# Performance work log

Measured on AMD Instinct MI355X. Metric: run time of the kernel, lower is better.

Reference implementation:

```python
import jax, jax.numpy as jnp
import numpy as np

N_NODES = 100
F_IN = 65536
C_OUT = 60
ACTION_DIM = 100
N_EDGES = 2000


def setup_inputs() -> dict:
    key = jax.random.key(0)
    ks = jax.random.split(key, 16)
    s = 0.02
    return {
        "substrate_features": jax.random.normal(ks[0], (1, N_NODES, F_IN), jnp.float32),
        "edge_index": jax.random.randint(ks[1], (2, N_EDGES), 0, N_NODES, dtype=jnp.int32),
        "v_cpu_demand_t": jax.random.uniform(ks[2], (1,), jnp.float32),
        "v_bw_demand_t": jax.random.uniform(ks[3], (1,), jnp.float32),
        "num_pending_v_nodes_t": jax.random.uniform(ks[4], (1,), jnp.float32),
        "actor_w": jax.random.normal(ks[5], (3, F_IN, C_OUT), jnp.float32) * s,
        "actor_b": jax.random.normal(ks[6], (C_OUT,), jnp.float32) * s,
        "critic_w": jax.random.normal(ks[7], (3, F_IN, C_OUT), jnp.float32) * s,
        "critic_b": jax.random.normal(ks[8], (C_OUT,), jnp.float32) * s,
        "actor_fc_w": jax.random.normal(ks[9], (N_NODES * C_OUT + 3, ACTION_DIM), jnp.float32) * s,
        "actor_fc_b": jax.random.normal(ks[10], (ACTION_DIM,), jnp.float32) * s,
        "critic_fc_w": jax.random.normal(ks[11], (N_NODES * C_OUT + 3, 1), jnp.float32) * s,
        "critic_fc_b": jax.random.normal(ks[12], (1,), jnp.float32) * s,
    }


def cheb_conv(x, edge_index, W, b):
    # ChebConv, K=3, sym normalization, lambda_max=2 (PyG defaults).
    # With lambda_max=2 the scaled Laplacian is L_hat = -D^{-1/2} A D^{-1/2}
    # (diagonal becomes 0 after the -1 self-loop shift).
    # x: [1, N, F]; edge_index: [2, E]; W: [3, F, C]; b: [C]
    src, dst = edge_index[0], edge_index[1]
    n = x.shape[1]
    deg = jax.ops.segment_sum(jnp.ones(src.shape[0], x.dtype), src, num_segments=n)
    dis = jnp.where(deg > 0, jax.lax.rsqrt(jnp.where(deg > 0, deg, 1.0)), 0.0)
    norm = -(dis[src] * dis[dst])  # [E], L_hat off-diagonal entries
    x2 = x[0]  # [N, F]

    def prop(z):  # z: [N, F] -> L_hat @ z via gather/scatter over edges
        return jax.ops.segment_sum(z[src] * norm[:, None], dst, num_segments=n)

    Tx0 = x2
    Tx1 = prop(Tx0)
    Tx2 = 2.0 * prop(Tx1) - Tx0
    out = Tx0 @ W[0] + Tx1 @ W[1] + Tx2 @ W[2] + b  # [N, C]
    return out[None]  # [1, N, C]


def reference(substrate_features, edge_index, v_cpu_demand_t, v_bw_demand_t,
              num_pending_v_nodes_t, actor_w, actor_b, critic_w, critic_b,
              actor_fc_w, actor_fc_b, critic_fc_w, critic_fc_b):
    emb_a = jnp.tanh(cheb_conv(substrate_features, edge_index, actor_w, actor_b))
    emb_a = emb_a.reshape(1, -1)  # [1, N*60]
    emb_c = jnp.tanh(cheb_conv(substrate_features, edge_index, critic_w, critic_b))
    emb_c = emb_c.reshape(1, -1)
    extras = [v_cpu_demand_t[None], v_bw_demand_t[None], num_pending_v_nodes_t[None]]  # each [1,1]
    state_a = jnp.concatenate([emb_a] + extras, axis=1)  # [1, 6003]
    state_c = jnp.concatenate([emb_c] + extras, axis=1)
    logits = state_a @ actor_fc_w + actor_fc_b  # [1, action_dim]
    values = state_c @ critic_fc_w + critic_fc_b  # [1, 1]
    return (logits, values)
```

## Files before the change

kernel.cpp:

```cpp
#include <hip/hip_runtime.h>
#include <stdint.h>

#define F_IN 65536
#define NN 100
#define CO 60
#define G_SPLIT 128
#define KC (F_IN/G_SPLIT)
#define BK 32
#define NIT (KC/BK)
#define NBUF 3
#define ABYTES (112*BK*2)
#define WBYTES (BK*CO*4)
#define BUFB (ABYTES+WBYTES)

typedef short v8s __attribute__((ext_vector_type(8)));
typedef float v4f __attribute__((ext_vector_type(4)));

__device__ __forceinline__ unsigned int f2bf(float x){
  unsigned int u = __float_as_uint(x);
  u += 0x7fffu + ((u>>16)&1u);
  return u>>16;
}
__device__ __forceinline__ v4f mfma16(v8s a, v8s b, v4f c){
  return __builtin_amdgcn_mfma_f32_16x16x32_bf16(a,b,c,0,0,0);
}
__device__ __forceinline__ void cp16(const void* g, void* l){
  __builtin_amdgcn_global_load_lds((const __attribute__((address_space(1))) void*)g,
                                   (__attribute__((address_space(3))) void*)l, 16, 0, 0);
}

__global__ __launch_bounds__(256)
void k_cvt(const float* __restrict__ x, unsigned short* __restrict__ xb){
  int i = blockIdx.x*256 + threadIdx.x;
  float4 v = ((const float4*)x)[i];
  uint2 w;
  w.x = f2bf(v.x) | (f2bf(v.y)<<16);
  w.y = f2bf(v.z) | (f2bf(v.w)<<16);
  ((uint2*)xb)[i] = w;
}

__global__ __launch_bounds__(256,3)
void k_gemm(const unsigned short* __restrict__ xb, const float* __restrict__ aw,
            const float* __restrict__ cw, float* __restrict__ dst, int partial){
  const int s = blockIdx.x, g = blockIdx.y;
  const int k0 = s*KC;
  const int tid = threadIdx.x, wave = tid>>6, lane = tid&63, quad = lane>>4, nl = lane&15;
  const int c0 = wave*16, ccl = min(c0+nl, CO-1);

  __shared__ __align__(16) char S[NBUF*BUFB];

  const float* W = (g<3) ? (aw + (size_t)g*F_IN*CO) : (cw + (size_t)(g-3)*F_IN*CO);

  const char* gsrc[4]; unsigned ldst[4]; unsigned gstep[4];
  #pragma unroll
  for(int i=0;i<4;++i){
    int id = wave*4 + i;
    if(id >= 15) id = 0;
    if(id < 7){
      int t = id;
      int row = t*16 + (lane>>2);
      int rcl = min(row, NN-1);
      int lch = (lane&3) ^ (row&3);
      gsrc[i]  = (const char*)(xb + (size_t)rcl*F_IN + k0) + lch*16;
      gstep[i] = BK*2;
      ldst[i]  = t*1024 + lane*16;
    } else {
      int t = id - 7;
      int off = t*1024; if(off > WBYTES-1024) off = WBYTES-1024;
      gsrc[i]  = (const char*)W + (size_t)k0*CO*4 + off + lane*16;
      gstep[i] = WBYTES;
      ldst[i]  = ABYTES + off + lane*16;
    }
  }

  v4f acc[7];
  #pragma unroll
  for(int i=0;i<7;++i){ v4f z={0.f,0.f,0.f,0.f}; acc[i]=z; }

  #define ISSUE(it) { char* b_ = S + ((it)%NBUF)*BUFB; \
    _Pragma("unroll") for(int i_=0;i_<4;++i_) cp16(gsrc[i_] + (size_t)(it)*gstep[i_], b_ + ldst[i_]); }

  #define COMPUTE(it) { const char* b_ = S + ((it)%NBUF)*BUFB; \
    const unsigned short* Ab_ = (const unsigned short*)b_; \
    const float* Wb_ = (const float*)(b_ + ABYTES); \
    v8s fB_; \
    _Pragma("unroll") for(int j_=0;j_<8;++j_) fB_[j_] = (short)f2bf(Wb_[(quad*8+j_)*CO + ccl]); \
    _Pragma("unroll") for(int mt_=0;mt_<7;++mt_){ \
      int r_ = mt_*16 + nl; \
      v8s a_ = *(const v8s*)(Ab_ + r_*BK + ((quad ^ (r_&3))*8)); \
      acc[mt_] = mfma16(a_, fB_, acc[mt_]); } }

  ISSUE(0); ISSUE(1);
  for(int it=0; it<NIT-1; ++it){
    __builtin_amdgcn_sched_barrier(0);
    asm volatile("s_waitcnt vmcnt(4)" ::: "memory");
    __builtin_amdgcn_s_barrier();
    __builtin_amdgcn_sched_barrier(0);
    if(it+2 < NIT) ISSUE(it+2);
    COMPUTE(it);
  }
  __builtin_amdgcn_sched_barrier(0);
  asm volatile("s_waitcnt vmcnt(0)" ::: "memory");
  __builtin_amdgcn_s_barrier();
  __builtin_amdgcn_sched_barrier(0);
  COMPUTE(NIT-1);

  const int c = c0 + nl;
  if(c < CO){
    if(partial){
      float* pd = dst + ((size_t)g*G_SPLIT + s)*(NN*CO);
      #pragma unroll
      for(int mt=0;mt<7;++mt){
        #pragma unroll
        for(int i=0;i<4;++i){
          int m = mt*16 + quad*4 + i;
          if(m < NN) pd[m*CO + c] = acc[mt][i];
        }
      }
    } else {
      float* pd = dst + (size_t)g*(NN*CO);
      #pragma unroll
      for(int mt=0;mt<7;++mt){
        #pragma unroll
        for(int i=0;i<4;++i){
          int m = mt*16 + quad*4 + i;
          if(m < NN) atomicAdd(pd + m*CO + c, acc[mt][i]);
        }
      }
    }
  }
}

__global__ void k_reduce(const float* __restrict__ P, float* __restrict__ Y){
  int o = blockIdx.x*256 + threadIdx.x;
  if(o >= 6*NN*CO) return;
  int gg = o/(NN*CO), r = o - gg*(NN*CO);
  const float* p = P + (size_t)gg*G_SPLIT*(NN*CO) + (size_t)blockIdx.y*32*(NN*CO) + r;
  float a0=0.f,a1=0.f,a2=0.f,a3=0.f;
  #pragma unroll 2
  for(int s4=0;s4<32;s4+=4){
    a0 += p[(s4  )*(NN*CO)];
    a1 += p[(s4+1)*(NN*CO)];
    a2 += p[(s4+2)*(NN*CO)];
    a3 += p[(s4+3)*(NN*CO)];
  }
  atomicAdd(&Y[o], (a0+a1)+(a2+a3));
}

__global__ void k_cheb(const float* __restrict__ Y, const int* __restrict__ ei,
                       const float* __restrict__ ab, const float* __restrict__ cb,
                       float* __restrict__ emb){
  const int net = blockIdx.x / CO;
  const int c   = blockIdx.x % CO;
  const int t   = threadIdx.x;
  __shared__ float L[NN][NN+1];
  __shared__ float dis[NN];
  __shared__ int   deg[NN];
  __shared__ float y0[NN], y1[NN], y2[NN], zu[NN];

  for(int i=t;i<NN*(NN+1);i+=128) ((float*)L)[i]=0.f;
  if(t<NN) deg[t]=0;
  __syncthreads();
  for(int e=t;e<2000;e+=128) atomicAdd(&deg[ei[e]],1);
  __syncthreads();
  if(t<NN) dis[t] = deg[t]>0 ? rsqrtf((float)deg[t]) : 0.f;
  __syncthreads();
  for(int e=t;e<2000;e+=128){
    int s = ei[e], d = ei[2000+e];
    atomicAdd(&L[d][s], -dis[s]*dis[d]);
  }
  if(t<NN){
    const float* yb = Y + (size_t)net*3*NN*CO + t*CO + c;
    y0[t]=yb[0]; y1[t]=yb[NN*CO]; y2[t]=yb[2*NN*CO];
  }
  __syncthreads();
  if(t<NN){
    float s=0.f;
    #pragma unroll 4
    for(int j=0;j<NN;++j) s += L[t][j]*y2[j];
    zu[t] = y1[t] + 2.f*s;
  }
  __syncthreads();
  if(t<NN){
    float s=0.f;
    #pragma unroll 4
    for(int j=0;j<NN;++j) s += L[t][j]*zu[j];
    float b = (net==0) ? ab[c] : cb[c];
    emb[net*NN*CO + t*CO + c] = tanhf(y0[t] - y2[t] + s + b);
  }
}

#define FCB 25
__global__ void k_fc(const float* __restrict__ emb, const float* __restrict__ afw,
                     const float* __restrict__ afb, const float* __restrict__ cfw,
                     const float* __restrict__ cfb, const float* __restrict__ s0,
                     const float* __restrict__ s1, const float* __restrict__ s2,
                     float* __restrict__ out){
  const int b = blockIdx.x;
  const int t = threadIdx.x;
  if(b < FCB){
    const int jj = t & 127, half = t >> 7;
    if(jj < 100){
      const int i0 = b*240 + half*120;
      const float* w = afw + (size_t)i0*100 + jj;
      const float* e = emb + i0;
      float p = 0.f;
      #pragma unroll 4
      for(int i=0;i<120;++i) p += e[i]*w[(size_t)i*100];
      atomicAdd(&out[jj], p);
    }
  } else {
    float p = 0.f;
    const float* e = emb + 6000;
    for(int i=t;i<6000;i+=256) p += e[i]*cfw[i];
    #pragma unroll
    for(int o=32;o>0;o>>=1) p += __shfl_down(p,o,64);
    __shared__ float red[4];
    if((t&63)==0) red[t>>6]=p;
    __syncthreads();
    if(t==0){
      float tot = red[0]+red[1]+red[2]+red[3];
      out[100] = tot + s0[0]*cfw[6000] + s1[0]*cfw[6001] + s2[0]*cfw[6002] + cfb[0];
    }
    if(t<100){
      atomicAdd(&out[t], afb[t] + s0[0]*afw[600000+t] + s1[0]*afw[600100+t] + s2[0]*afw[600200+t]);
    }
  }
}

extern "C" void kernel_launch(void* const* d_in, const int* in_sizes, int n_in,
                              void* d_out, int out_size, void* d_ws, size_t ws_size,
                              hipStream_t stream){
  const float* x   = (const float*)d_in[0];
  const int*   ei  = (const int*)d_in[1];
  const float* s0  = (const float*)d_in[2];
  const float* s1  = (const float*)d_in[3];
  const float* s2  = (const float*)d_in[4];
  const float* aw  = (const float*)d_in[5];
  const float* ab  = (const float*)d_in[6];
  const float* cw  = (const float*)d_in[7];
  const float* cb  = (const float*)d_in[8];
  const float* afw = (const float*)d_in[9];
  const float* afb = (const float*)d_in[10];
  const float* cfw = (const float*)d_in[11];
  const float* cfb = (const float*)d_in[12];
  float* out = (float*)d_out;

  unsigned short* xb = (unsigned short*)d_ws;
  float* Y   = (float*)((char*)d_ws + 13107200);
  float* emb = Y + 6*NN*CO;
  float* P   = emb + 2*NN*CO;
  const size_t need_full = 13107200u + (size_t)(6*NN*CO + 2*NN*CO)*4 + (size_t)6*G_SPLIT*NN*CO*4;
  const int partial = (ws_size >= need_full) ? 1 : 0;

  hipMemsetAsync(Y, 0, 6*NN*CO*sizeof(float), stream);
  hipMemsetAsync(out, 0, 101*sizeof(float), stream);

  k_cvt<<<6400, 256, 0, stream>>>(x, xb);
  k_gemm<<<dim3(G_SPLIT,6), 256, 0, stream>>>(xb, aw, cw, partial ? P : Y, partial);
  if(partial){
    k_reduce<<<dim3((6*NN*CO+255)/256, 4), 256, 0, stream>>>(P, Y);
  }
  k_cheb<<<120, 128, 0, stream>>>(Y, ei, ab, cb, emb);
  k_fc<<<FCB+1, 256, 0, stream>>>(emb, afw, afb, cfw, cfb, s0, s1, s2, out);
}
```

Before: 218.8 us.

## Replace LDS-staged GEMM pipeline with direct global loads and double the K split

Drops the triple-buffered global_load_lds staging of activations and weights in the split-K GEMM. Each lane now loads its A fragments and W column values straight from global memory into registers. The K split doubles to 256 slices, so twice as many blocks each run a shorter loop, occupancy hint rises to 4, and the reduce grid grows to match. This removes LDS traffic and barriers, but gives up explicit prefetch and coalesced weight loads: each lane reads 8 strided floats per step. It also doubles the partial-sum buffer and the reduce work.

```diff
diff --git a/kernel.cpp b/kernel.cpp
--- a/kernel.cpp
+++ b/kernel.cpp
@@ -4,14 +4,10 @@
 #define F_IN 65536
 #define NN 100
 #define CO 60
-#define G_SPLIT 128
+#define G_SPLIT 256
 #define KC (F_IN/G_SPLIT)
 #define BK 32
 #define NIT (KC/BK)
-#define NBUF 3
-#define ABYTES (112*BK*2)
-#define WBYTES (BK*CO*4)
-#define BUFB (ABYTES+WBYTES)
 
 typedef short v8s __attribute__((ext_vector_type(8)));
 typedef float v4f __attribute__((ext_vector_type(4)));
@@ -23,10 +19,6 @@
 }
 __device__ __forceinline__ v4f mfma16(v8s a, v8s b, v4f c){
   return __builtin_amdgcn_mfma_f32_16x16x32_bf16(a,b,c,0,0,0);
-}
-__device__ __forceinline__ void cp16(const void* g, void* l){
-  __builtin_amdgcn_global_load_lds((const __attribute__((address_space(1))) void*)g,
-                                   (__attribute__((address_space(3))) void*)l, 16, 0, 0);
 }
 
 __global__ __launch_bounds__(256)
@@ -39,7 +31,7 @@
   ((uint2*)xb)[i] = w;
 }
 
-__global__ __launch_bounds__(256,3)
+__global__ __launch_bounds__(256,4)
 void k_gemm(const unsigned short* __restrict__ xb, const float* __restrict__ aw,
             const float* __restrict__ cw, float* __restrict__ dst, int partial){
   const int s = blockIdx.x, g = blockIdx.y;
@@ -47,63 +39,43 @@
   const int tid = threadIdx.x, wave = tid>>6, lane = tid&63, quad = lane>>4, nl = lane&15;
   const int c0 = wave*16, ccl = min(c0+nl, CO-1);
 
-  __shared__ __align__(16) char S[NBUF*BUFB];
-
-  const float* W = (g<3) ? (aw + (size_t)g*F_IN*CO) : (cw + (size_t)(g-3)*F_IN*CO);
-
-  const char* gsrc[4]; unsigned ldst[4]; unsigned gstep[4];
+  const float* Wm = (g<3) ? (aw + (size_t)g*F_IN*CO) : (cw + (size_t)(g-3)*F_IN*CO);
+  const float* wp = Wm + (size_t)(k0 + quad*8)*CO + ccl;
+
+  const unsigned short* ap[7];
   #pragma unroll
-  for(int i=0;i<4;++i){
-    int id = wave*4 + i;
-    if(id >= 15) id = 0;
-    if(id < 7){
-      int t = id;
-      int row = t*16 + (lane>>2);
-      int rcl = min(row, NN-1);
-      int lch = (lane&3) ^ (row&3);
-      gsrc[i]  = (const char*)(xb + (size_t)rcl*F_IN + k0) + lch*16;
-      gstep[i] = BK*2;
-      ldst[i]  = t*1024 + lane*16;
-    } else {
-      int t = id - 7;
-      int off = t*1024; if(off > WBYTES-1024) off = WBYTES-1024;
-      gsrc[i]  = (const char*)W + (size_t)k0*CO*4 + off + lane*16;
-      gstep[i] = WBYTES;
-      ldst[i]  = ABYTES + off + lane*16;
-    }
+  for(int mt=0;mt<7;++mt){
+    int r = mt*16 + nl;
+    int rcl = min(r, NN-1);
+    ap[mt] = xb + (size_t)rcl*F_IN + k0 + quad*8;
   }
 
   v4f acc[7];
   #pragma unroll
   for(int i=0;i<7;++i){ v4f z={0.f,0.f,0.f,0.f}; acc[i]=z; }
 
-  #define ISSUE(it) { char* b_ = S + ((it)%NBUF)*BUFB; \
-    _Pragma("unroll") for(int i_=0;i_<4;++i_) cp16(gsrc[i_] + (size_t)(it)*gstep[i_], b_ + ldst[i_]); }
-
-  #define COMPUTE(it) { const char* b_ = S + ((it)%NBUF)*BUFB; \
-    const unsigned short* Ab_ = (const unsigned short*)b_; \
-    const float* Wb_ = (const float*)(b_ + ABYTES); \
-    v8s fB_; \
-    _Pragma("unroll") for(int j_=0;j_<8;++j_) fB_[j_] = (short)f2bf(Wb_[(quad*8+j_)*CO + ccl]); \
-    _Pragma("unroll") for(int mt_=0;mt_<7;++mt_){ \
-      int r_ = mt_*16 + nl; \
-      v8s a_ = *(const v8s*)(Ab_ + r_*BK + ((quad ^ (r_&3))*8)); \
-      acc[mt_] = mfma16(a_, fB_, acc[mt_]); } }
-
-  ISSUE(0); ISSUE(1);
-  for(int it=0; it<NIT-1; ++it){
-    __builtin_amdgcn_sched_barrier(0);
-    asm volatile("s_waitcnt vmcnt(4)" ::: "memory");
-    __builtin_amdgcn_s_barrier();
-    __builtin_amdgcn_sched_barrier(0);
-    if(it+2 < NIT) ISSUE(it+2);
-    COMPUTE(it);
-  }
-  __builtin_amdgcn_sched_barrier(0);
-  asm volatile("s_waitcnt vmcnt(0)" ::: "memory");
-  __builtin_amdgcn_s_barrier();
-  __builtin_amdgcn_sched_barrier(0);
-  COMPUTE(NIT-1);
+  for(int it=0; it<NIT; ++it){
+    const int kk = it*BK;
+    v8s a0 = *(const v8s*)(ap[0] + kk);
+    v8s a1 = *(const v8s*)(ap[1] + kk);
+    v8s a2 = *(const v8s*)(ap[2] + kk);
+    v8s a3 = *(const v8s*)(ap[3] + kk);
+    v8s a4 = *(const v8s*)(ap[4] + kk);
+    v8s a5 = *(const v8s*)(ap[5] + kk);
+    v8s a6 = *(const v8s*)(ap[6] + kk);
+    float w0 = wp[(kk+0)*CO], w1 = wp[(kk+1)*CO], w2 = wp[(kk+2)*CO], w3 = wp[(kk+3)*CO];
+    float w4 = wp[(kk+4)*CO], w5 = wp[(kk+5)*CO], w6 = wp[(kk+6)*CO], w7 = wp[(kk+7)*CO];
+    v8s fB;
+    fB[0]=(short)f2bf(w0); fB[1]=(short)f2bf(w1); fB[2]=(short)f2bf(w2); fB[3]=(short)f2bf(w3);
+    fB[4]=(short)f2bf(w4); fB[5]=(short)f2bf(w5); fB[6]=(short)f2bf(w6); fB[7]=(short)f2bf(w7);
+    acc[0] = mfma16(a0, fB, acc[0]);
+    acc[1] = mfma16(a1, fB, acc[1]);
+    acc[2] = mfma16(a2, fB, acc[2]);
+    acc[3] = mfma16(a3, fB, acc[3]);
+    acc[4] = mfma16(a4, fB, acc[4]);
+    acc[5] = mfma16(a5, fB, acc[5]);
+    acc[6] = mfma16(a6, fB, acc[6]);
+  }
 
   const int c = c0 + nl;
   if(c < CO){
@@ -250,7 +222,8 @@
   float* Y   = (float*)((char*)d_ws + 13107200);
   float* emb = Y + 6*NN*CO;
   float* P   = emb + 2*NN*CO;
-  const size_t need_full = 13107200u + (size_t)(6*NN*CO + 2*NN*CO)*4 + (size_t)6*G_SPLIT*NN*CO*4;
+  const size_t need_full = 13107200u + (size_t)(6*NN*CO + 2*NN*CO)*4
+                         + (size_t)6*G_SPLIT*NN*CO*4;
   const int partial = (ws_size >= need_full) ? 1 : 0;
 
   hipMemsetAsync(Y, 0, 6*NN*CO*sizeof(float), stream);
@@ -259,7 +232,7 @@
   k_cvt<<<6400, 256, 0, stream>>>(x, xb);
   k_gemm<<<dim3(G_SPLIT,6), 256, 0, stream>>>(xb, aw, cw, partial ? P : Y, partial);
   if(partial){
-    k_reduce<<<dim3((6*NN*CO+255)/256, 4), 256, 0, stream>>>(P, Y);
+    k_reduce<<<dim3((6*NN*CO+255)/256, 8), 256, 0, stream>>>(P, Y);
   }
   k_cheb<<<120, 128, 0, stream>>>(Y, ei, ab, cb, emb);
   k_fc<<<FCB+1, 256, 0, stream>>>(emb, afw, afb, cfw, cfb, s0, s1, s2, out);
```

Measured after the change: 243.3 us. +11.2%, slower.
